# Optimization experiments

Hardware: AMD Instinct MI355X
Metric: run time of the kernel (lower is better)

The kernel has to match this reference:

```python
import jax, jax.numpy as jnp
import numpy as np

N, E, B = 100000, 3200000, 64   # nodes, edges, graphs
F_IN, F_OUT, N_OUT = 20, 20, 5


def setup_inputs() -> dict:
    key = jax.random.key(0)
    ks = jax.random.split(key, 9)
    x = jax.random.normal(ks[0], (N, F_IN), jnp.float32)
    edge_index = jax.random.randint(ks[1], (2, E), 0, N, dtype=jnp.int32)
    batch = jnp.sort(jax.random.randint(ks[2], (N,), 0, B, dtype=jnp.int32))
    s = 1.0 / np.sqrt(F_IN)
    W = jax.random.normal(ks[3], (F_IN, F_OUT), jnp.float32) * s       # GAT linear
    att_src = jax.random.normal(ks[4], (F_OUT,), jnp.float32) * s      # a_src (heads=1)
    att_dst = jax.random.normal(ks[5], (F_OUT,), jnp.float32) * s      # a_dst
    bias = jax.random.normal(ks[6], (F_OUT,), jnp.float32) * 0.01
    out_W = jax.random.normal(ks[7], (F_OUT, N_OUT), jnp.float32) * s
    out_b = jax.random.normal(ks[8], (N_OUT,), jnp.float32) * 0.01
    return {"x": x, "edge_index": edge_index, "batch": batch, "W": W,
            "att_src": att_src, "att_dst": att_dst, "bias": bias,
            "out_W": out_W, "out_b": out_b}


def reference(x, edge_index, batch, W, att_src, att_dst, bias, out_W, out_b):
    n = x.shape[0]
    # PyG GATConv default: add self-loops
    loop = jnp.arange(n, dtype=edge_index.dtype)
    src = jnp.concatenate([edge_index[0], loop])
    dst = jnp.concatenate([edge_index[1], loop])

    h = x @ W                                   # [N, F_OUT]
    a_s = h @ att_src                           # [N]
    a_d = h @ att_dst                           # [N]
    # per-edge attention logit, LeakyReLU(0.2) as in PyG GATConv
    e = jax.nn.leaky_relu(a_s[src] + a_d[dst], negative_slope=0.2)
    # segment softmax over incoming edges of each destination node
    m = jax.ops.segment_max(e, dst, num_segments=n)
    ex = jnp.exp(e - m[dst])
    den = jax.ops.segment_sum(ex, dst, num_segments=n)
    alpha = ex / den[dst]                       # [E+N]  (dropout inactive in eval)
    agg = jax.ops.segment_sum(alpha[:, None] * h[src], dst, num_segments=n) + bias

    xact = jax.nn.leaky_relu(agg, negative_slope=0.01)   # nn.LeakyReLU default
    # global mean pool per graph
    cnt = jax.ops.segment_sum(jnp.ones((n,), xact.dtype), batch, num_segments=B)
    pooled = jax.ops.segment_sum(xact, batch, num_segments=B) / jnp.maximum(cnt, 1.0)[:, None]
    logits = pooled @ out_W + out_b             # [B, 5]
    return jax.nn.softmax(logits, axis=-1)
```

## Files before the change

### kernel.cpp

```cpp
#include <hip/hip_runtime.h>
#include <math.h>

#define F_IN 20
#define F_OUT 20
#define N_OUT 5
#define NPB 128
#define NPB_SH 7
#define NBLK_A 256
#define HSW 16
#define CAPMAX 5632
#define NBUCKMAX 800
#define SPMAX 8

__device__ __forceinline__ unsigned pack2bf(float a, float b) {
    unsigned ua = __float_as_uint(a);
    unsigned ub = __float_as_uint(b);
    ua = (ua + 0x7fffu + ((ua >> 16) & 1u)) >> 16;
    ub = ((ub + 0x7fffu + ((ub >> 16) & 1u)) >> 16) << 16;
    return ua | ub;
}
#define BF2LO(u) __uint_as_float((u) << 16)
#define BF2HI(u) __uint_as_float((u) & 0xffff0000u)

__global__ __launch_bounds__(1024) void k1a_fused(
    const float* __restrict__ x, const float* __restrict__ W,
    const float* __restrict__ att_s, const float* __restrict__ att_d,
    unsigned* __restrict__ hpack, float* __restrict__ a_d,
    const int* __restrict__ ei, int* __restrict__ gcur,
    unsigned int* __restrict__ bdata,
    int n, int E, int nbuck, int cap, int k1blocks)
{
    __shared__ float sW[F_IN * F_OUT];
    __shared__ float sas[F_OUT];
    __shared__ float sad[F_OUT];
    __shared__ int   sh[3 * NBUCKMAX];

    int tid = threadIdx.x;

    if (blockIdx.x < k1blocks) {
        for (int i = tid; i < F_IN * F_OUT; i += 1024) sW[i] = W[i];
        if (tid < F_OUT) { sas[tid] = att_s[tid]; sad[tid] = att_d[tid]; }
        __syncthreads();

        int i = blockIdx.x * 1024 + tid;
        if (i >= n) return;

        float xi[F_IN];
        const float4* xp = (const float4*)(x + (size_t)i * F_IN);
#pragma unroll
        for (int q = 0; q < F_IN / 4; ++q) {
            float4 v = xp[q];
            xi[4 * q + 0] = v.x; xi[4 * q + 1] = v.y;
            xi[4 * q + 2] = v.z; xi[4 * q + 3] = v.w;
        }

        float hrow[F_OUT];
        float as_acc = 0.f, ad_acc = 0.f;
#pragma unroll
        for (int j = 0; j < F_OUT; ++j) {
            float hj = 0.f;
#pragma unroll
            for (int k = 0; k < F_IN; ++k) hj += xi[k] * sW[k * F_OUT + j];
            hrow[j] = hj;
            as_acc += hj * sas[j];
            ad_acc += hj * sad[j];
        }

        unsigned rw[HSW];
#pragma unroll
        for (int j = 0; j < 10; ++j) rw[j] = pack2bf(hrow[2 * j], hrow[2 * j + 1]);
        rw[10] = __float_as_uint(as_acc);
#pragma unroll
        for (int j = 11; j < HSW; ++j) rw[j] = 0u;

        uint4* hp = (uint4*)(hpack + (size_t)i * HSW);
#pragma unroll
        for (int q = 0; q < HSW / 4; ++q) {
            uint4 v;
            v.x = rw[4 * q + 0]; v.y = rw[4 * q + 1];
            v.z = rw[4 * q + 2]; v.w = rw[4 * q + 3];
            hp[q] = v;
        }
        a_d[i] = ad_acc;
    } else {
        int bb   = blockIdx.x - k1blocks;
        int nbb  = gridDim.x - k1blocks;
        int* hist = sh;
        int* base = sh + nbuck;
        int* cur  = sh + 2 * nbuck;
        for (int b = tid; b < nbuck; b += 1024) { hist[b] = 0; cur[b] = 0; }
        __syncthreads();

        int chunk = (E + nbb - 1) / nbb;
        int start = bb * chunk;
        int end   = min(E, start + chunk);
        const int* dsts = ei + E;

        for (int e = start + tid; e < end; e += 1024)
            atomicAdd(&hist[dsts[e] >> NPB_SH], 1);
        __syncthreads();

        for (int b = tid; b < nbuck; b += 1024) {
            int c = hist[b];
            base[b] = c ? atomicAdd(&gcur[b], c) : 0;
        }
        __syncthreads();

        for (int e = start + tid; e < end; e += 1024) {
            int d = dsts[e];
            int s = ei[e];
            int b = d >> NPB_SH;
            int pos = base[b] + atomicAdd(&cur[b], 1);
            if (pos < cap)
                bdata[(size_t)b * cap + pos] =
                    ((unsigned)s << NPB_SH) | (unsigned)(d & (NPB - 1));
        }
    }
}

__global__ __launch_bounds__(512) void kb_srt(const int* __restrict__ gcur,
                                              const unsigned int* __restrict__ bdata,
                                              const unsigned* __restrict__ hpack,
                                              const float* __restrict__ a_d,
                                              const float* __restrict__ bias,
                                              const int* __restrict__ batch,
                                              float* __restrict__ pooled,
                                              int n, int cap)
{
    __shared__ int   sent[CAPMAX];
    __shared__ int   hist[NPB];
    __shared__ int   incl[NPB];
    __shared__ int   cur[NPB];
    __shared__ float adl[NPB];
    __shared__ int   sbatch[NPB];
    __shared__ float sbias[F_OUT];
    __shared__ float spool[SPMAX * F_OUT];

    int b = blockIdx.x;
    int node_lo = b << NPB_SH;
    int nn = min(NPB, n - node_lo);
    int tid = threadIdx.x;

    if (tid < NPB) { hist[tid] = 0; cur[tid] = 0; }
    if (tid < nn) {
        adl[tid] = a_d[node_lo + tid];
        sbatch[tid] = batch[node_lo + tid];
    }
    if (tid < F_OUT) sbias[tid] = bias[tid];
    if (tid < SPMAX * F_OUT) spool[tid] = 0.f;
    __syncthreads();

    int cnt = min(gcur[b], cap);
    const unsigned int* bd = bdata + (size_t)b * cap;

    for (int e = tid; e < cnt; e += 512)
        atomicAdd(&hist[bd[e] & (NPB - 1)], 1);
    __syncthreads();

    if (tid < NPB) incl[tid] = hist[tid];
    __syncthreads();
#pragma unroll
    for (int s = 1; s < NPB; s <<= 1) {
        int v = 0;
        if (tid < NPB && tid >= s) v = incl[tid - s];
        __syncthreads();
        if (tid < NPB) incl[tid] += v;
        __syncthreads();
    }

    for (int e = tid; e < cnt; e += 512) {
        unsigned w = bd[e];
        int ldst = (int)(w & (NPB - 1));
        int pos = incl[ldst] - hist[ldst] + atomicAdd(&cur[ldst], 1);
        sent[pos] = (int)(w >> NPB_SH);
    }
    __syncthreads();

    int node = tid >> 2, sub = tid & 3;
    float acc[21];
#pragma unroll
    for (int f = 0; f < 21; ++f) acc[f] = 0.f;

    if (node < nn) {
        int start = incl[node] - hist[node];
        int end   = incl[node];
        float ad  = adl[node];
        for (int k = start + sub; k < end; k += 4) {
            int src = sent[k];
            const uint4* rp = (const uint4*)(hpack + (size_t)src * HSW);
            uint4 r0 = rp[0], r1 = rp[1], r2 = rp[2];
            float as = __uint_as_float(r2.z);
            float vv = as + ad;
            vv = vv > 0.f ? vv : 0.2f * vv;
            float ex = __expf(vv);
            acc[0]  += ex * BF2LO(r0.x); acc[1]  += ex * BF2HI(r0.x);
            acc[2]  += ex * BF2LO(r0.y); acc[3]  += ex * BF2HI(r0.y);
            acc[4]  += ex * BF2LO(r0.z); acc[5]  += ex * BF2HI(r0.z);
            acc[6]  += ex * BF2LO(r0.w); acc[7]  += ex * BF2HI(r0.w);
            acc[8]  += ex * BF2LO(r1.x); acc[9]  += ex * BF2HI(r1.x);
            acc[10] += ex * BF2LO(r1.y); acc[11] += ex * BF2HI(r1.y);
            acc[12] += ex * BF2LO(r1.z); acc[13] += ex * BF2HI(r1.z);
            acc[14] += ex * BF2LO(r1.w); acc[15] += ex * BF2HI(r1.w);
            acc[16] += ex * BF2LO(r2.x); acc[17] += ex * BF2HI(r2.x);
            acc[18] += ex * BF2LO(r2.y); acc[19] += ex * BF2HI(r2.y);
            acc[20] += ex;
        }
    }

#pragma unroll
    for (int f = 0; f < 21; ++f) {
        acc[f] += __shfl_xor(acc[f], 1);
        acc[f] += __shfl_xor(acc[f], 2);
    }

    if (node < nn && sub == 0) {
        int i = node_lo + node;
        const uint4* rp = (const uint4*)(hpack + (size_t)i * HSW);
        uint4 r0 = rp[0], r1 = rp[1], r2 = rp[2];
        float vv = __uint_as_float(r2.z) + adl[node];
        vv = vv > 0.f ? vv : 0.2f * vv;
        float exs = __expf(vv);
        float inv = 1.f / (acc[20] + exs);

        float hs[F_OUT];
        hs[0]  = BF2LO(r0.x); hs[1]  = BF2HI(r0.x);
        hs[2]  = BF2LO(r0.y); hs[3]  = BF2HI(r0.y);
        hs[4]  = BF2LO(r0.z); hs[5]  = BF2HI(r0.z);
        hs[6]  = BF2LO(r0.w); hs[7]  = BF2HI(r0.w);
        hs[8]  = BF2LO(r1.x); hs[9]  = BF2HI(r1.x);
        hs[10] = BF2LO(r1.y); hs[11] = BF2HI(r1.y);
        hs[12] = BF2LO(r1.z); hs[13] = BF2HI(r1.z);
        hs[14] = BF2LO(r1.w); hs[15] = BF2HI(r1.w);
        hs[16] = BF2LO(r2.x); hs[17] = BF2HI(r2.x);
        hs[18] = BF2LO(r2.y); hs[19] = BF2HI(r2.y);

        float v[F_OUT];
#pragma unroll
        for (int f = 0; f < F_OUT; ++f) {
            float t = (acc[f] + exs * hs[f]) * inv + sbias[f];
            v[f] = t > 0.f ? t : 0.01f * t;
        }

        int gl = sbatch[node] - sbatch[0];
        if (gl < SPMAX) {
#pragma unroll
            for (int f = 0; f < F_OUT; ++f) atomicAdd(&spool[gl * F_OUT + f], v[f]);
        } else {
#pragma unroll
            for (int f = 0; f < F_OUT; ++f)
                atomicAdd(&pooled[(size_t)sbatch[node] * F_OUT + f], v[f]);
        }
    }
    __syncthreads();

    int g0 = sbatch[0];
    int ngl = min(SPMAX, sbatch[nn - 1] - g0 + 1);
    for (int idx = tid; idx < ngl * F_OUT; idx += 512)
        atomicAdd(&pooled[(size_t)(g0 + idx / F_OUT) * F_OUT + idx % F_OUT], spool[idx]);
}

__global__ void k4_head(const float* __restrict__ pooled, const int* __restrict__ batch,
                        const float* __restrict__ out_W, const float* __restrict__ out_b,
                        float* __restrict__ out, int B, int n)
{
    int g = blockIdx.x * blockDim.x + threadIdx.x;
    if (g >= B) return;

    int bnd[2];
#pragma unroll
    for (int t = 0; t < 2; ++t) {
        int target = g + t;
        int lo = 0, hi = n;
        while (lo < hi) {
            int m = (lo + hi) >> 1;
            if (batch[m] < target) lo = m + 1; else hi = m;
        }
        bnd[t] = lo;
    }
    float cntf = (float)(bnd[1] - bnd[0]);
    float invc = 1.f / (cntf > 1.f ? cntf : 1.f);

    float p[F_OUT];
#pragma unroll
    for (int f = 0; f < F_OUT; ++f) p[f] = pooled[(size_t)g * F_OUT + f] * invc;

    float lg[N_OUT];
#pragma unroll
    for (int o = 0; o < N_OUT; ++o) {
        float acc = out_b[o];
#pragma unroll
        for (int f = 0; f < F_OUT; ++f) acc += p[f] * out_W[f * N_OUT + o];
        lg[o] = acc;
    }
    float m = lg[0];
#pragma unroll
    for (int o = 1; o < N_OUT; ++o) m = lg[o] > m ? lg[o] : m;
    float s = 0.f;
#pragma unroll
    for (int o = 0; o < N_OUT; ++o) { lg[o] = expf(lg[o] - m); s += lg[o]; }
    float inv = 1.f / s;
#pragma unroll
    for (int o = 0; o < N_OUT; ++o) out[g * N_OUT + o] = lg[o] * inv;
}

extern "C" void kernel_launch(void* const* d_in, const int* in_sizes, int n_in,
                              void* d_out, int out_size, void* d_ws, size_t ws_size,
                              hipStream_t stream)
{
    const float* x       = (const float*)d_in[0];
    const int*   ei      = (const int*)  d_in[1];
    const int*   batch   = (const int*)  d_in[2];
    const float* W       = (const float*)d_in[3];
    const float* att_src = (const float*)d_in[4];
    const float* att_dst = (const float*)d_in[5];
    const float* bias    = (const float*)d_in[6];
    const float* out_W   = (const float*)d_in[7];
    const float* out_b   = (const float*)d_in[8];
    float* out = (float*)d_out;

    int n = in_sizes[0] / F_IN;
    int E = in_sizes[1] / 2;
    int B = out_size / N_OUT;

    int nbuck = (n + NPB - 1) >> NPB_SH;
    int avg   = E / nbuck;
    int cap   = avg + avg / 4 + 256;
    if (cap > CAPMAX) cap = CAPMAX;

    char* ws = (char*)d_ws;
    unsigned* hpack = (unsigned*)ws;   ws += (size_t)n * HSW * 4;
    float* a_d      = (float*)ws;      ws += (size_t)n * 4;
    int*   gcur     = (int*)ws;        ws += (size_t)nbuck * 4;
    float* pooled   = (float*)ws;      ws += (size_t)B * F_OUT * 4;
    ws = (char*)(((size_t)ws + 15) & ~(size_t)15);
    unsigned int* bdata = (unsigned int*)ws;  ws += (size_t)nbuck * cap * 4;

    hipMemsetAsync(gcur, 0, (size_t)nbuck * 4 + (size_t)B * F_OUT * 4, stream);

    int k1blocks = (n + 1023) / 1024;

    k1a_fused<<<k1blocks + NBLK_A, 1024, 0, stream>>>(
        x, W, att_src, att_dst, hpack, a_d, ei, gcur, bdata,
        n, E, nbuck, cap, k1blocks);
    kb_srt   <<<nbuck, 512, 0, stream>>>(gcur, bdata, hpack, a_d, bias, batch,
                                         pooled, n, cap);
    k4_head  <<<1, 64, 0, stream>>>(pooled, batch, out_W, out_b, out, B, n);
}
```

Measured before the change: 197.9 us.

## Stage edge binning in shared memory for coalesced bucket writes, halve bucket size

The binning blocks now sort each fixed-size edge chunk by destination bucket in shared memory, using a local histogram and prefix scan, before writing to global memory. Each bucket's run is then written contiguously, replacing scattered per-edge stores with runs of consecutive addresses. Buckets shrink from 128 to 64 nodes, which doubles the bucket count and halves the per-block work in the aggregation kernel, now launched with 256 threads. The cost is extra shared-memory passes, a scan with many barriers, and a binary search per element when writing out.

```diff
diff --git a/kernel.cpp b/kernel.cpp
--- a/kernel.cpp
+++ b/kernel.cpp
@@ -4,13 +4,13 @@
 #define F_IN 20
 #define F_OUT 20
 #define N_OUT 5
-#define NPB 128
-#define NPB_SH 7
-#define NBLK_A 256
+#define NPB 64
+#define NPB_SH 6
 #define HSW 16
-#define CAPMAX 5632
-#define NBUCKMAX 800
-#define SPMAX 8
+#define CAPMAX 2816
+#define NBINMAX 1600
+#define CHUNK 13056
+#define SPMAX 4
 
 __device__ __forceinline__ unsigned pack2bf(float a, float b) {
     unsigned ua = __float_as_uint(a);
@@ -30,16 +30,17 @@
     unsigned int* __restrict__ bdata,
     int n, int E, int nbuck, int cap, int k1blocks)
 {
-    __shared__ float sW[F_IN * F_OUT];
-    __shared__ float sas[F_OUT];
-    __shared__ float sad[F_OUT];
-    __shared__ int   sh[3 * NBUCKMAX];
+    __shared__ union {
+        struct { float sW[F_IN * F_OUT]; float sas[F_OUT]; float sad[F_OUT]; } lin;
+        struct { int hist[NBINMAX]; int incl[NBINMAX]; int curb[NBINMAX];
+                 unsigned sbuf[CHUNK]; } bin;
+    } u;
 
     int tid = threadIdx.x;
 
     if (blockIdx.x < k1blocks) {
-        for (int i = tid; i < F_IN * F_OUT; i += 1024) sW[i] = W[i];
-        if (tid < F_OUT) { sas[tid] = att_s[tid]; sad[tid] = att_d[tid]; }
+        for (int i = tid; i < F_IN * F_OUT; i += 1024) u.lin.sW[i] = W[i];
+        if (tid < F_OUT) { u.lin.sas[tid] = att_s[tid]; u.lin.sad[tid] = att_d[tid]; }
         __syncthreads();
 
         int i = blockIdx.x * 1024 + tid;
@@ -60,10 +61,10 @@
         for (int j = 0; j < F_OUT; ++j) {
             float hj = 0.f;
 #pragma unroll
-            for (int k = 0; k < F_IN; ++k) hj += xi[k] * sW[k * F_OUT + j];
+            for (int k = 0; k < F_IN; ++k) hj += xi[k] * u.lin.sW[k * F_OUT + j];
             hrow[j] = hj;
-            as_acc += hj * sas[j];
-            ad_acc += hj * sad[j];
+            as_acc += hj * u.lin.sas[j];
+            ad_acc += hj * u.lin.sad[j];
         }
 
         unsigned rw[HSW];
@@ -83,42 +84,68 @@
         }
         a_d[i] = ad_acc;
     } else {
-        int bb   = blockIdx.x - k1blocks;
-        int nbb  = gridDim.x - k1blocks;
-        int* hist = sh;
-        int* base = sh + nbuck;
-        int* cur  = sh + 2 * nbuck;
-        for (int b = tid; b < nbuck; b += 1024) { hist[b] = 0; cur[b] = 0; }
-        __syncthreads();
-
-        int chunk = (E + nbb - 1) / nbb;
-        int start = bb * chunk;
-        int end   = min(E, start + chunk);
+        int bb    = blockIdx.x - k1blocks;
+        int start = bb * CHUNK;
+        int chunk = min(CHUNK, E - start);
+        if (chunk <= 0) return;
         const int* dsts = ei + E;
 
-        for (int e = start + tid; e < end; e += 1024)
-            atomicAdd(&hist[dsts[e] >> NPB_SH], 1);
+        for (int b = tid; b < nbuck; b += 1024) { u.bin.hist[b] = 0; u.bin.curb[b] = 0; }
+        __syncthreads();
+
+        for (int e = tid; e < chunk; e += 1024)
+            atomicAdd(&u.bin.hist[dsts[start + e] >> NPB_SH], 1);
+        __syncthreads();
+
+        int b0 = 2 * tid, b1 = 2 * tid + 1;
+        int h0 = (b0 < nbuck) ? u.bin.hist[b0] : 0;
+        int h1 = (b1 < nbuck) ? u.bin.hist[b1] : 0;
+        int psum = h0 + h1;
+        u.bin.incl[tid] = psum;
+        __syncthreads();
+        for (int s = 1; s < 1024; s <<= 1) {
+            int v = (tid >= s) ? u.bin.incl[tid - s] : 0;
+            __syncthreads();
+            u.bin.incl[tid] += v;
+            __syncthreads();
+        }
+        int excl = u.bin.incl[tid] - psum;
+        __syncthreads();
+        if (b0 < nbuck) u.bin.incl[b0] = excl + h0;
+        if (b1 < nbuck) u.bin.incl[b1] = excl + h0 + h1;
+        __syncthreads();
+
+        for (int e = tid; e < chunk; e += 1024) {
+            int d = dsts[start + e];
+            int s = ei[start + e];
+            int b = d >> NPB_SH;
+            int pos = u.bin.incl[b] - u.bin.hist[b] + atomicAdd(&u.bin.curb[b], 1);
+            u.bin.sbuf[pos] = ((unsigned)s << NPB_SH) | (unsigned)(d & (NPB - 1));
+        }
         __syncthreads();
 
         for (int b = tid; b < nbuck; b += 1024) {
-            int c = hist[b];
-            base[b] = c ? atomicAdd(&gcur[b], c) : 0;
-        }
-        __syncthreads();
-
-        for (int e = start + tid; e < end; e += 1024) {
-            int d = dsts[e];
-            int s = ei[e];
-            int b = d >> NPB_SH;
-            int pos = base[b] + atomicAdd(&cur[b], 1);
-            if (pos < cap)
-                bdata[(size_t)b * cap + pos] =
-                    ((unsigned)s << NPB_SH) | (unsigned)(d & (NPB - 1));
-        }
-    }
-}
-
-__global__ __launch_bounds__(512) void kb_srt(const int* __restrict__ gcur,
+            int c = u.bin.hist[b];
+            u.bin.curb[b] = c ? atomicAdd(&gcur[b], c) : 0;
+        }
+        __syncthreads();
+
+        for (int p = tid; p < chunk; p += 1024) {
+            unsigned w = u.bin.sbuf[p];
+            int lo = 0, hi = nbuck;
+            while (lo < hi) {
+                int m = (lo + hi) >> 1;
+                if (u.bin.incl[m] <= p) lo = m + 1; else hi = m;
+            }
+            int b  = lo;
+            int st = u.bin.incl[b] - u.bin.hist[b];
+            int gpos = u.bin.curb[b] + (p - st);
+            if (gpos < cap) bdata[(size_t)b * cap + gpos] = w;
+        }
+    }
+}
+
+__global__ __launch_bounds__(256) void kb_srt(const int* __restrict__ gcur,
                                               const unsigned int* __restrict__ bdata,
                                               const unsigned* __restrict__ hpack,
                                               const float* __restrict__ a_d,
@@ -153,7 +180,7 @@
     int cnt = min(gcur[b], cap);
     const unsigned int* bd = bdata + (size_t)b * cap;
 
-    for (int e = tid; e < cnt; e += 512)
+    for (int e = tid; e < cnt; e += 256)
         atomicAdd(&hist[bd[e] & (NPB - 1)], 1);
     __syncthreads();
 
@@ -168,7 +195,7 @@
         __syncthreads();
     }
 
-    for (int e = tid; e < cnt; e += 512) {
+    for (int e = tid; e < cnt; e += 256) {
         unsigned w = bd[e];
         int ldst = (int)(w & (NPB - 1));
         int pos = incl[ldst] - hist[ldst] + atomicAdd(&cur[ldst], 1);
@@ -255,7 +282,7 @@
 
     int g0 = sbatch[0];
     int ngl = min(SPMAX, sbatch[nn - 1] - g0 + 1);
-    for (int idx = tid; idx < ngl * F_OUT; idx += 512)
+    for (int idx = tid; idx < ngl * F_OUT; idx += 256)
         atomicAdd(&pooled[(size_t)(g0 + idx / F_OUT) * F_OUT + idx % F_OUT], spool[idx]);
 }
 
@@ -338,11 +365,12 @@
     hipMemsetAsync(gcur, 0, (size_t)nbuck * 4 + (size_t)B * F_OUT * 4, stream);
 
     int k1blocks = (n + 1023) / 1024;
-
-    k1a_fused<<<k1blocks + NBLK_A, 1024, 0, stream>>>(
+    int nbb      = (E + CHUNK - 1) / CHUNK;
+
+    k1a_fused<<<k1blocks + nbb, 1024, 0, stream>>>(
         x, W, att_src, att_dst, hpack, a_d, ei, gcur, bdata,
         n, E, nbuck, cap, k1blocks);
-    kb_srt   <<<nbuck, 512, 0, stream>>>(gcur, bdata, hpack, a_d, bias, batch,
+    kb_srt   <<<nbuck, 256, 0, stream>>>(gcur, bdata, hpack, a_d, bias, batch,
                                          pooled, n, cap);
     k4_head  <<<1, 64, 0, stream>>>(pooled, batch, out_W, out_b, out, B, n);
 }
```

Measured after the change: 178.4 us. -9.9%, faster.
